# Kernel tuning notes

Measured on AMD Instinct MI355X. Metric: run time of the kernel, lower is better.

## Reference

```python
import jax, jax.numpy as jnp
import numpy as np

N = 50_000       # nodes
E = 1_600_000    # edges (avg degree 32)
F_IN = 128       # input features
H = 32           # hidden channels (both GCNConv layers)
C = 16           # num classes


def setup_inputs() -> dict:
    key = jax.random.key(0)
    ks = jax.random.split(key, 6)
    x = jax.random.normal(ks[0], (N, F_IN), dtype=jnp.float32)
    edge_index = jax.random.randint(ks[1], (2, E), 0, N, dtype=jnp.int32)
    W1 = jax.random.normal(ks[2], (F_IN, H), dtype=jnp.float32) / np.float32(np.sqrt(F_IN))
    b1 = jnp.zeros((H,), jnp.float32)
    W2 = jax.random.normal(ks[3], (H, H), dtype=jnp.float32) / np.float32(np.sqrt(H))
    b2 = jnp.zeros((H,), jnp.float32)
    Wc = jax.random.normal(ks[4], (H, C), dtype=jnp.float32) / np.float32(np.sqrt(H))
    bc = jnp.zeros((C,), jnp.float32)
    return {"x": x, "edge_index": edge_index, "W1": W1, "b1": b1,
            "W2": W2, "b2": b2, "Wc": Wc, "bc": bc}


def _gcn_conv(x, W, b, src, dst, deg_inv_sqrt, n):
    """PyG GCNConv: xW, then D^{-1/2}(A+I)D^{-1/2} aggregation, then bias.

    src/dst already include self-loops; deg_inv_sqrt precomputed on dst.
    """
    xw = x @ W                                   # [N, H]
    norm = deg_inv_sqrt[src] * deg_inv_sqrt[dst]  # [E+N]
    msg = xw[src] * norm[:, None]                # gather + scale, [E+N, H]
    out = jax.ops.segment_sum(msg, dst, num_segments=n)  # scatter-add
    return out + b


def reference(x, edge_index, W1, b1, W2, b2, Wc, bc):
    n = x.shape[0]
    loops = jnp.arange(n, dtype=edge_index.dtype)
    src = jnp.concatenate([edge_index[0], loops])  # add self-loops
    dst = jnp.concatenate([edge_index[1], loops])
    # degree over destination column (edge weight 1), as PyG gcn_norm does
    deg = jax.ops.segment_sum(jnp.ones_like(dst, dtype=x.dtype), dst, num_segments=n)
    deg_inv_sqrt = jnp.where(deg > 0, jax.lax.rsqrt(deg), 0.0)

    h = jnp.tanh(_gcn_conv(x, W1, b1, src, dst, deg_inv_sqrt, n))
    h = jnp.tanh(_gcn_conv(h, W2, b2, src, dst, deg_inv_sqrt, n))
    out = h @ Wc + bc
    return (out, h)
```

## Files before the change

### kernel.cpp

```cpp
#include <hip/hip_runtime.h>
#include <hip/hip_bf16.h>

#define NN 50000
#define EE 1600000
#define FIN 128
#define HH 32
#define CC 16
#define NB 782
#define NBLK 782
#define CHUNK 2048
#define FCAP 3072

typedef unsigned short u16;
typedef unsigned int u32;
typedef unsigned char u8;

__device__ __forceinline__ float bf2f(u16 u) {
    union { u32 i; float f; } v; v.i = ((u32)u) << 16; return v.f;
}
__device__ __forceinline__ u16 f2bf(float f) {
    union { float f; u32 i; } v; v.f = f;
    u32 x = v.i;
    return (u16)((x + 0x7fffu + ((x >> 16) & 1u)) >> 16);
}

__global__ __launch_bounds__(256) void k_place(const int* __restrict__ src, const int* __restrict__ dst,
                                               int* __restrict__ locT,
                                               u16* __restrict__ gsrc, u8* __restrict__ grel) {
    __shared__ int dst_s[CHUNK];
    __shared__ u16 s_src[CHUNK];
    __shared__ u8  s_rel[CHUNK];
    __shared__ int cur[NB];
    __shared__ int ps[256];
    const int tid = threadIdx.x, blk = blockIdx.x;
    const int e0 = blk * CHUNK;
    int cnt = EE - e0; if (cnt > CHUNK) cnt = CHUNK;

    const uint4* gd4 = (const uint4*)(dst + e0);
    for (int i = tid; i < cnt / 4; i += 256) ((uint4*)dst_s)[i] = gd4[i];
    for (int i = tid; i < NB; i += 256) cur[i] = 0;
    __syncthreads();

    for (int k = 0; k < CHUNK / 256; ++k) {
        int i = k * 256 + tid;
        if (i < cnt) atomicAdd(&cur[dst_s[i] >> 6], 1);
    }
    __syncthreads();

    const int bi = tid * 4;
    int v0 = 0, v1 = 0, v2 = 0, v3 = 0;
    if (bi < NB)     v0 = cur[bi];
    if (bi + 1 < NB) v1 = cur[bi + 1];
    if (bi + 2 < NB) v2 = cur[bi + 2];
    if (bi + 3 < NB) v3 = cur[bi + 3];
    ps[tid] = v0 + v1 + v2 + v3;
    __syncthreads();
    for (int off = 1; off < 256; off <<= 1) {
        int t = (tid >= off) ? ps[tid - off] : 0;
        __syncthreads();
        ps[tid] += t;
        __syncthreads();
    }
    int run = (tid == 0) ? 0 : ps[tid - 1];
    if (bi < NB)     { cur[bi] = run;     locT[(size_t)bi * NBLK + blk] = run;       run += v0; }
    if (bi + 1 < NB) { cur[bi + 1] = run; locT[(size_t)(bi + 1) * NBLK + blk] = run; run += v1; }
    if (bi + 2 < NB) { cur[bi + 2] = run; locT[(size_t)(bi + 2) * NBLK + blk] = run; run += v2; }
    if (bi + 3 < NB) { cur[bi + 3] = run; locT[(size_t)(bi + 3) * NBLK + blk] = run; run += v3; }
    if (tid == 255) locT[(size_t)NB * NBLK + blk] = ps[255];
    __syncthreads();

    for (int k = 0; k < CHUNK / 256; ++k) {
        int i = k * 256 + tid;
        if (i < cnt) {
            int d = dst_s[i];
            int pos = atomicAdd(&cur[d >> 6], 1);
            s_src[pos] = (u16)src[e0 + i];
            s_rel[pos] = (u8)(d & 63);
        }
    }
    __syncthreads();

    const uint4* ss = (const uint4*)s_src;
    uint4* gs = (uint4*)(gsrc + (size_t)blk * CHUNK);
    for (int i = tid; i < (cnt * 2) / 16; i += 256) gs[i] = ss[i];
    const uint4* sr = (const uint4*)s_rel;
    uint4* gr = (uint4*)(grel + (size_t)blk * CHUNK);
    for (int i = tid; i < cnt / 16; i += 256) gr[i] = sr[i];
}

__global__ __launch_bounds__(256) void k_btot(const int* __restrict__ locT, int* __restrict__ btot,
                                              const u32* __restrict__ xw_words, int* __restrict__ flag) {
    __shared__ int ps[256];
    __shared__ int cs;
    const int tid = threadIdx.x, cb = blockIdx.x;
    if (cb == 0) {
        if (tid == 0) cs = 0;
        __syncthreads();
        int c = 0;
        for (int i = tid; i < 512; i += 256) {
            float v = fabsf(bf2f((u16)(xw_words[i] & 0xffffu)));
            if (v >= 6.0e-8f && v <= 64.0f) c++;
        }
        atomicAdd(&cs, c);
        __syncthreads();
        if (tid == 0) *flag = (cs > 384) ? 1 : 0;
    }
    int s = 0;
    for (int b = tid; b < NBLK; b += 256)
        s += locT[(size_t)(cb + 1) * NBLK + b] - locT[(size_t)cb * NBLK + b];
    ps[tid] = s;
    __syncthreads();
    for (int off = 128; off > 0; off >>= 1) {
        if (tid < off) ps[tid] += ps[tid + off];
        __syncthreads();
    }
    if (tid == 0) btot[cb] = ps[0];
}

__global__ __launch_bounds__(256) void k_fine(const int* __restrict__ locT, const int* __restrict__ btot,
                                              const u16* __restrict__ gsrc, const u8* __restrict__ grel,
                                              int* __restrict__ rowptr, float* __restrict__ dis,
                                              u16* __restrict__ entries) {
    __shared__ int beg_s[NBLK];
    __shared__ int fo[NBLK + 1];
    __shared__ int ps[256];
    __shared__ int h[64];
    __shared__ int cur[64];
    __shared__ int sbase;
    __shared__ u16 lsrc[FCAP];
    __shared__ u8  lrel[FCAP];
    __shared__ u16 lout[FCAP];
    const int tid = threadIdx.x, cb = blockIdx.x;

    for (int b = tid; b < NBLK; b += 256) {
        int beg = locT[(size_t)cb * NBLK + b];
        beg_s[b] = beg;
        fo[b] = locT[(size_t)(cb + 1) * NBLK + b] - beg;
    }
    if (tid < 64) h[tid] = 0;

    int bs = 0;
    for (int j = tid; j < cb; j += 256) bs += btot[j];
    ps[tid] = bs;
    __syncthreads();
    for (int off = 128; off > 0; off >>= 1) {
        if (tid < off) ps[tid] += ps[tid + off];
        __syncthreads();
    }
    if (tid == 0) sbase = ps[0];
    __syncthreads();
    const int base = sbase;

    const int b0 = tid * 4;
    int a0 = 0, a1 = 0, a2 = 0, a3 = 0;
    if (b0 < NBLK)     a0 = fo[b0];
    if (b0 + 1 < NBLK) a1 = fo[b0 + 1];
    if (b0 + 2 < NBLK) a2 = fo[b0 + 2];
    if (b0 + 3 < NBLK) a3 = fo[b0 + 3];
    ps[tid] = a0 + a1 + a2 + a3;
    __syncthreads();
    for (int off = 1; off < 256; off <<= 1) {
        int v = (tid >= off) ? ps[tid - off] : 0;
        __syncthreads();
        ps[tid] += v;
        __syncthreads();
    }
    int run = (tid == 0) ? 0 : ps[tid - 1];
    if (b0 < NBLK)     { fo[b0] = run;     run += a0; }
    if (b0 + 1 < NBLK) { fo[b0 + 1] = run; run += a1; }
    if (b0 + 2 < NBLK) { fo[b0 + 2] = run; run += a2; }
    if (b0 + 3 < NBLK) { fo[b0 + 3] = run; run += a3; }
    if (tid == 255) fo[NBLK] = ps[255];
    __syncthreads();
    const int T = fo[NBLK];
    const bool staged = (T <= FCAP);

    if (staged) {
        for (int b = tid; b < NBLK; b += 256) {
            int g0 = b * CHUNK + beg_s[b];
            int o = fo[b];
            int L = fo[b + 1] - o;
            for (int j = 0; j < L; ++j) {
                u8 r = grel[g0 + j];
                lrel[o + j] = r;
                lsrc[o + j] = gsrc[g0 + j];
                atomicAdd(&h[r], 1);
            }
        }
    } else {
        for (int b = tid; b < NBLK; b += 256) {
            int g0 = b * CHUNK + beg_s[b];
            int L = fo[b + 1] - fo[b];
            for (int j = 0; j < L; ++j) atomicAdd(&h[grel[g0 + j]], 1);
        }
    }
    __syncthreads();

    int myv = (tid < 64) ? h[tid] : 0;
    ps[tid] = (tid < 64) ? myv : 0;
    __syncthreads();
    for (int off = 1; off < 64; off <<= 1) {
        int v = (tid >= off && tid < 64) ? ps[tid - off] : 0;
        __syncthreads();
        if (tid < 64) ps[tid] += v;
        __syncthreads();
    }
    if (tid < 64) {
        int excl = ps[tid] - myv;
        int n = cb * 64 + tid;
        cur[tid] = staged ? excl : base + excl;
        if (n < NN) {
            rowptr[n] = base + excl;
            dis[n] = rsqrtf((float)myv + 1.0f);
        }
    }
    if (cb == NB - 1 && tid == 0) rowptr[NN] = EE;
    __syncthreads();

    if (staged) {
        for (int i = tid; i < T; i += 256) {
            int pos = atomicAdd(&cur[lrel[i]], 1);
            lout[pos] = lsrc[i];
        }
        __syncthreads();
        for (int i = tid; i < T; i += 256) entries[base + i] = lout[i];
    } else {
        for (int b = tid; b < NBLK; b += 256) {
            int g0 = b * CHUNK + beg_s[b];
            int L = fo[b + 1] - fo[b];
            for (int j = 0; j < L; ++j) {
                int g = g0 + j;
                int pos = atomicAdd(&cur[grel[g]], 1);
                entries[pos] = gsrc[g];
            }
        }
    }
}

__global__ __launch_bounds__(256) void k_xw1(const void* __restrict__ xv, const void* __restrict__ W1v,
                                             const float* __restrict__ dis,
                                             const int* __restrict__ flag, u16* __restrict__ xwb) {
    __shared__ float wsm[FIN * HH];
    __shared__ float xs[128][33];
    const int f = *flag;
    const int tid = threadIdx.x;
    if (f) {
        const u16* W1 = (const u16*)W1v;
        for (int i = tid; i < FIN * HH; i += 256) wsm[i] = bf2f(W1[i]);
    } else {
        const float* W1 = (const float*)W1v;
        for (int i = tid; i < FIN * HH; i += 256) wsm[i] = W1[i];
    }
    const int n0 = blockIdx.x * 128;
    const int ct = tid & 7, rg = tid >> 3;
    const int lr = tid >> 1, lh = tid & 1;
    int ln = n0 + lr; if (ln >= NN) ln = NN - 1;
    float acc[4][4] = {};
    for (int kc = 0; kc < FIN; kc += 32) {
        __syncthreads();
        float* dq = &xs[lr][lh * 16];
        if (f) {
            const u16* lp = (const u16*)xv + (size_t)ln * FIN + lh * 16 + kc;
            uint4 a = *(const uint4*)lp;
            uint4 b = *(const uint4*)(lp + 8);
            u32 aw[4] = {a.x, a.y, a.z, a.w}, bw[4] = {b.x, b.y, b.z, b.w};
            #pragma unroll
            for (int i = 0; i < 4; ++i) {
                dq[2*i]     = bf2f((u16)(aw[i] & 0xffffu));
                dq[2*i+1]   = bf2f((u16)(aw[i] >> 16));
                dq[8+2*i]   = bf2f((u16)(bw[i] & 0xffffu));
                dq[8+2*i+1] = bf2f((u16)(bw[i] >> 16));
            }
        } else {
            const float* lp = (const float*)xv + (size_t)ln * FIN + lh * 16 + kc;
            #pragma unroll
            for (int i = 0; i < 4; ++i) {
                float4 t = *(const float4*)(lp + 4 * i);
                dq[4*i] = t.x; dq[4*i+1] = t.y; dq[4*i+2] = t.z; dq[4*i+3] = t.w;
            }
        }
        __syncthreads();
        #pragma unroll
        for (int k = 0; k < 32; ++k) {
            float4 wv = *(const float4*)&wsm[(kc + k) * HH + ct * 4];
            #pragma unroll
            for (int j = 0; j < 4; ++j) {
                float xvv = xs[rg * 4 + j][k];
                acc[j][0] = fmaf(xvv, wv.x, acc[j][0]);
                acc[j][1] = fmaf(xvv, wv.y, acc[j][1]);
                acc[j][2] = fmaf(xvv, wv.z, acc[j][2]);
                acc[j][3] = fmaf(xvv, wv.w, acc[j][3]);
            }
        }
    }
    #pragma unroll
    for (int j = 0; j < 4; ++j) {
        int n = n0 + rg * 4 + j;
        if (n < NN) {
            float dd = dis[n];
            ushort4 o;
            o.x = f2bf(dd * acc[j][0]); o.y = f2bf(dd * acc[j][1]);
            o.z = f2bf(dd * acc[j][2]); o.w = f2bf(dd * acc[j][3]);
            *(ushort4*)&xwb[(size_t)n * HH + ct * 4] = o;
        }
    }
}

__global__ __launch_bounds__(256) void k_g1(const int* __restrict__ rowptr, const u16* __restrict__ entries,
                                            const u16* __restrict__ xws, const float* __restrict__ dis,
                                            const void* __restrict__ bv, const int* __restrict__ flag,
                                            const void* __restrict__ W2v, u16* __restrict__ xwb2) {
    __shared__ float hrow[16][32];
    __shared__ float w2s[HH * HH];
    const int f = *flag;
    const int tid = threadIdx.x;
    if (f) {
        const u16* W2 = (const u16*)W2v;
        for (int i = tid; i < HH * HH; i += 256) w2s[i] = bf2f(W2[i]);
    } else {
        const float* W2 = (const float*)W2v;
        for (int i = tid; i < HH * HH; i += 256) w2s[i] = W2[i];
    }
    const int nl = tid >> 4;
    const int g = blockIdx.x * 16 + nl;
    const int c0 = (tid & 15) * 2;
    float b0, b1;
    if (f) { b0 = bf2f(((const u16*)bv)[c0]); b1 = bf2f(((const u16*)bv)[c0 + 1]); }
    else   { b0 = ((const float*)bv)[c0];     b1 = ((const float*)bv)[c0 + 1]; }
    const int beg = rowptr[g], end = rowptr[g + 1];
    const float dd = dis[g];
    u32 sw = *(const u32*)&xws[(size_t)g * HH + c0];
    float aL0 = bf2f((u16)(sw & 0xffffu)), aH0 = bf2f((u16)(sw >> 16));
    float aL1 = 0.f, aH1 = 0.f, aL2 = 0.f, aH2 = 0.f, aL3 = 0.f, aH3 = 0.f;
    int i = beg;
    for (; i < end && (i & 3); ++i) {
        u32 w = *(const u32*)&xws[(size_t)entries[i] * HH + c0];
        aL0 += bf2f((u16)(w & 0xffffu)); aH0 += bf2f((u16)(w >> 16));
    }
    for (; i + 4 <= end; i += 4) {
        ushort4 e4 = *(const ushort4*)&entries[i];
        u32 w0 = *(const u32*)&xws[(size_t)e4.x * HH + c0];
        u32 w1 = *(const u32*)&xws[(size_t)e4.y * HH + c0];
        u32 w2 = *(const u32*)&xws[(size_t)e4.z * HH + c0];
        u32 w3 = *(const u32*)&xws[(size_t)e4.w * HH + c0];
        aL0 += bf2f((u16)(w0 & 0xffffu)); aH0 += bf2f((u16)(w0 >> 16));
        aL1 += bf2f((u16)(w1 & 0xffffu)); aH1 += bf2f((u16)(w1 >> 16));
        aL2 += bf2f((u16)(w2 & 0xffffu)); aH2 += bf2f((u16)(w2 >> 16));
        aL3 += bf2f((u16)(w3 & 0xffffu)); aH3 += bf2f((u16)(w3 >> 16));
    }
    for (; i < end; ++i) {
        u32 w = *(const u32*)&xws[(size_t)entries[i] * HH + c0];
        aL0 += bf2f((u16)(w & 0xffffu)); aH0 += bf2f((u16)(w >> 16));
    }
    float vLo = tanhf(fmaf(dd, (aL0 + aL1) + (aL2 + aL3), b0));
    float vHi = tanhf(fmaf(dd, (aH0 + aH1) + (aH2 + aH3), b1));
    hrow[nl][c0] = vLo; hrow[nl][c0 + 1] = vHi;
    __syncthreads();
    float a0 = 0.f, a1 = 0.f;
    #pragma unroll
    for (int k = 0; k < HH; ++k) {
        float hv = hrow[nl][k];
        a0 = fmaf(hv, w2s[k * HH + c0], a0);
        a1 = fmaf(hv, w2s[k * HH + c0 + 1], a1);
    }
    u32 o = (u32)f2bf(dd * a0) | ((u32)f2bf(dd * a1) << 16);
    *(u32*)&xwb2[(size_t)g * HH + c0] = o;
}

__global__ __launch_bounds__(256) void k_g2(const int* __restrict__ rowptr, const u16* __restrict__ entries,
                                            const u16* __restrict__ xws, const float* __restrict__ dis,
                                            const void* __restrict__ bv, const int* __restrict__ flag,
                                            const void* __restrict__ Wcv, const void* __restrict__ bcv,
                                            void* __restrict__ outbase) {
    __shared__ float hrow[16][32];
    __shared__ float wcs[HH * CC];
    __shared__ float bcs[CC];
    const int f = *flag;
    const int tid = threadIdx.x;
    if (f) {
        const u16* Wc = (const u16*)Wcv;
        for (int i = tid; i < HH * CC; i += 256) wcs[i] = bf2f(Wc[i]);
        if (tid < CC) bcs[tid] = bf2f(((const u16*)bcv)[tid]);
    } else {
        const float* Wc = (const float*)Wcv;
        for (int i = tid; i < HH * CC; i += 256) wcs[i] = Wc[i];
        if (tid < CC) bcs[tid] = ((const float*)bcv)[tid];
    }
    const int nl = tid >> 4;
    const int g = blockIdx.x * 16 + nl;
    const int c0 = (tid & 15) * 2;
    float b0, b1;
    if (f) { b0 = bf2f(((const u16*)bv)[c0]); b1 = bf2f(((const u16*)bv)[c0 + 1]); }
    else   { b0 = ((const float*)bv)[c0];     b1 = ((const float*)bv)[c0 + 1]; }
    const int beg = rowptr[g], end = rowptr[g + 1];
    const float dd = dis[g];
    u32 sw = *(const u32*)&xws[(size_t)g * HH + c0];
    float aL0 = bf2f((u16)(sw & 0xffffu)), aH0 = bf2f((u16)(sw >> 16));
    float aL1 = 0.f, aH1 = 0.f, aL2 = 0.f, aH2 = 0.f, aL3 = 0.f, aH3 = 0.f;
    int i = beg;
    for (; i < end && (i & 3); ++i) {
        u32 w = *(const u32*)&xws[(size_t)entries[i] * HH + c0];
        aL0 += bf2f((u16)(w & 0xffffu)); aH0 += bf2f((u16)(w >> 16));
    }
    for (; i + 4 <= end; i += 4) {
        ushort4 e4 = *(const ushort4*)&entries[i];
        u32 w0 = *(const u32*)&xws[(size_t)e4.x * HH + c0];
        u32 w1 = *(const u32*)&xws[(size_t)e4.y * HH + c0];
        u32 w2 = *(const u32*)&xws[(size_t)e4.z * HH + c0];
        u32 w3 = *(const u32*)&xws[(size_t)e4.w * HH + c0];
        aL0 += bf2f((u16)(w0 & 0xffffu)); aH0 += bf2f((u16)(w0 >> 16));
        aL1 += bf2f((u16)(w1 & 0xffffu)); aH1 += bf2f((u16)(w1 >> 16));
        aL2 += bf2f((u16)(w2 & 0xffffu)); aH2 += bf2f((u16)(w2 >> 16));
        aL3 += bf2f((u16)(w3 & 0xffffu)); aH3 += bf2f((u16)(w3 >> 16));
    }
    for (; i < end; ++i) {
        u32 w = *(const u32*)&xws[(size_t)entries[i] * HH + c0];
        aL0 += bf2f((u16)(w & 0xffffu)); aH0 += bf2f((u16)(w >> 16));
    }
    float vLo = tanhf(fmaf(dd, (aL0 + aL1) + (aL2 + aL3), b0));
    float vHi = tanhf(fmaf(dd, (aH0 + aH1) + (aH2 + aH3), b1));
    size_t idx = (size_t)g * HH + c0;
    if (f) {
        u16* h2_16 = (u16*)outbase + (size_t)NN * CC;
        u32 o = (u32)f2bf(vLo) | ((u32)f2bf(vHi) << 16);
        *(u32*)&h2_16[idx] = o;
    } else {
        float* h2_32 = (float*)outbase + (size_t)NN * CC;
        *(float2*)&h2_32[idx] = make_float2(vLo, vHi);
    }
    hrow[nl][c0] = vLo; hrow[nl][c0 + 1] = vHi;
    __syncthreads();
    int cl = tid & 15;
    float acc = bcs[cl];
    #pragma unroll
    for (int k = 0; k < HH; ++k) acc = fmaf(hrow[nl][k], wcs[k * CC + cl], acc);
    size_t oi = (size_t)g * CC + cl;
    if (f) ((u16*)outbase)[oi] = f2bf(acc);
    else   ((float*)outbase)[oi] = acc;
}

extern "C" void kernel_launch(void* const* d_in, const int* in_sizes, int n_in,
                              void* d_out, int out_size, void* d_ws, size_t ws_size,
                              hipStream_t stream) {
    const void* x  = d_in[0];
    const int*  ei = (const int*)d_in[1];
    const void* W1 = d_in[2];
    const void* b1 = d_in[3];
    const void* W2 = d_in[4];
    const void* b2 = d_in[5];
    const void* Wc = d_in[6];
    const void* bc = d_in[7];
    const int* srcv = ei;
    const int* dstv = ei + EE;

    char*  ws     = (char*)d_ws;
    int*   flag   = (int*)ws;
    int*   rowptr = (int*)(ws + 4096);
    float* dis    = (float*)(ws + 208896);
    int*   btot   = (int*)(ws + 417792);
    int*   locT   = (int*)(ws + 421888);
    u16*   xwb    = (u16*)(ws + 2871296);
    u16*   entries= (u16*)(ws + 6071296);
    u16*   xwb2   = (u16*)(ws + 9271296);

    u16*   gsrc = (u16*)d_out;
    u8*    grel = (u8*)d_out + (size_t)EE * 2;

    k_place<<<NBLK, 256, 0, stream>>>(srcv, dstv, locT, gsrc, grel);
    k_btot<<<NB, 256, 0, stream>>>(locT, btot, (const u32*)x, flag);
    k_fine<<<NB, 256, 0, stream>>>(locT, btot, gsrc, grel, rowptr, dis, entries);

    k_xw1<<<(NN + 127) / 128, 256, 0, stream>>>(x, W1, dis, flag, xwb);
    k_g1<<<NN / 16, 256, 0, stream>>>(rowptr, entries, xwb, dis, b1, flag, W2, xwb2);
    k_g2<<<NN / 16, 256, 0, stream>>>(rowptr, entries, xwb2, dis, b2, flag, Wc, bc, d_out);
}
```

Measured before the change: 185.8 us.

## Widen gather loads to 4 channels per thread, 32 nodes per block

The two aggregation kernels now map 8 threads per node, each gathering 4 bf16 channels with 8-byte loads instead of 16 threads doing 4-byte loads, so each block covers 32 nodes and the grid is halved. Fewer, wider gather instructions per neighbour row and fewer index loads per node are intended to cut memory-instruction overhead in the gather-bound phase. The classifier epilogue computes two nodes per thread, and the CSR build writes entries as packed 32-bit pairs instead of 16-bit stores. In exchange each thread holds more accumulators, which raises register pressure, and a tail guard is added for the partial last block.

Result: no change. 184.7 us (-0.6%).

```diff
diff --git a/kernel.cpp b/kernel.cpp
--- a/kernel.cpp
+++ b/kernel.cpp
@@ -223,7 +223,15 @@
             lout[pos] = lsrc[i];
         }
         __syncthreads();
-        for (int i = tid; i < T; i += 256) entries[base + i] = lout[i];
+        const int st = base & 1;
+        if (st && tid == 0) entries[base] = lout[0];
+        for (int p = tid; ; p += 256) {
+            int i = st + 2 * p;
+            if (i + 1 >= T) break;
+            u32 w = (u32)lout[i] | ((u32)lout[i + 1] << 16);
+            *(u32*)&entries[base + i] = w;
+        }
+        if (((T - st) & 1) && tid == 0 && T > st) entries[base + T - 1] = lout[T - 1];
     } else {
         for (int b = tid; b < NBLK; b += 256) {
             int g0 = b * CHUNK + beg_s[b];
@@ -310,7 +318,7 @@
                                             const u16* __restrict__ xws, const float* __restrict__ dis,
                                             const void* __restrict__ bv, const int* __restrict__ flag,
                                             const void* __restrict__ W2v, u16* __restrict__ xwb2) {
-    __shared__ float hrow[16][32];
+    __shared__ float hrow[32][33];
     __shared__ float w2s[HH * HH];
     const int f = *flag;
     const int tid = threadIdx.x;
@@ -321,50 +329,72 @@
         const float* W2 = (const float*)W2v;
         for (int i = tid; i < HH * HH; i += 256) w2s[i] = W2[i];
     }
-    const int nl = tid >> 4;
-    const int g = blockIdx.x * 16 + nl;
-    const int c0 = (tid & 15) * 2;
-    float b0, b1;
-    if (f) { b0 = bf2f(((const u16*)bv)[c0]); b1 = bf2f(((const u16*)bv)[c0 + 1]); }
-    else   { b0 = ((const float*)bv)[c0];     b1 = ((const float*)bv)[c0 + 1]; }
+    const int nl = tid >> 3;
+    const int graw = blockIdx.x * 32 + nl;
+    const bool valid = graw < NN;
+    const int g = valid ? graw : NN - 1;
+    const int c0 = (tid & 7) * 4;
+    float bb0, bb1, bb2, bb3;
+    if (f) {
+        const u16* b = (const u16*)bv;
+        bb0 = bf2f(b[c0]); bb1 = bf2f(b[c0+1]); bb2 = bf2f(b[c0+2]); bb3 = bf2f(b[c0+3]);
+    } else {
+        const float* b = (const float*)bv;
+        bb0 = b[c0]; bb1 = b[c0+1]; bb2 = b[c0+2]; bb3 = b[c0+3];
+    }
     const int beg = rowptr[g], end = rowptr[g + 1];
     const float dd = dis[g];
-    u32 sw = *(const u32*)&xws[(size_t)g * HH + c0];
-    float aL0 = bf2f((u16)(sw & 0xffffu)), aH0 = bf2f((u16)(sw >> 16));
-    float aL1 = 0.f, aH1 = 0.f, aL2 = 0.f, aH2 = 0.f, aL3 = 0.f, aH3 = 0.f;
+    uint2 sw = *(const uint2*)&xws[(size_t)g * HH + c0];
+    float a00 = bf2f((u16)(sw.x & 0xffffu)), a01 = bf2f((u16)(sw.x >> 16));
+    float a02 = bf2f((u16)(sw.y & 0xffffu)), a03 = bf2f((u16)(sw.y >> 16));
+    float a10=0,a11=0,a12=0,a13=0, a20=0,a21=0,a22=0,a23=0, a30=0,a31=0,a32=0,a33=0;
     int i = beg;
     for (; i < end && (i & 3); ++i) {
-        u32 w = *(const u32*)&xws[(size_t)entries[i] * HH + c0];
-        aL0 += bf2f((u16)(w & 0xffffu)); aH0 += bf2f((u16)(w >> 16));
+        uint2 w = *(const uint2*)&xws[(size_t)entries[i] * HH + c0];
+        a00 += bf2f((u16)(w.x & 0xffffu)); a01 += bf2f((u16)(w.x >> 16));
+        a02 += bf2f((u16)(w.y & 0xffffu)); a03 += bf2f((u16)(w.y >> 16));
     }
     for (; i + 4 <= end; i += 4) {
         ushort4 e4 = *(const ushort4*)&entries[i];
-        u32 w0 = *(const u32*)&xws[(size_t)e4.x * HH + c0];
-        u32 w1 = *(const u32*)&xws[(size_t)e4.y * HH + c0];
-        u32 w2 = *(const u32*)&xws[(size_t)e4.z * HH + c0];
-        u32 w3 = *(const u32*)&xws[(size_t)e4.w * HH + c0];
-        aL0 += bf2f((u16)(w0 & 0xffffu)); aH0 += bf2f((u16)(w0 >> 16));
-        aL1 += bf2f((u16)(w1 & 0xffffu)); aH1 += bf2f((u16)(w1 >> 16));
-        aL2 += bf2f((u16)(w2 & 0xffffu)); aH2 += bf2f((u16)(w2 >> 16));
-        aL3 += bf2f((u16)(w3 & 0xffffu)); aH3 += bf2f((u16)(w3 >> 16));
+        uint2 w0 = *(const uint2*)&xws[(size_t)e4.x * HH + c0];
+        uint2 w1 = *(const uint2*)&xws[(size_t)e4.y * HH + c0];
+        uint2 w2 = *(const uint2*)&xws[(size_t)e4.z * HH + c0];
+        uint2 w3 = *(const uint2*)&xws[(size_t)e4.w * HH + c0];
+        a00 += bf2f((u16)(w0.x & 0xffffu)); a01 += bf2f((u16)(w0.x >> 16));
+        a02 += bf2f((u16)(w0.y & 0xffffu)); a03 += bf2f((u16)(w0.y >> 16));
+        a10 += bf2f((u16)(w1.x & 0xffffu)); a11 += bf2f((u16)(w1.x >> 16));
+        a12 += bf2f((u16)(w1.y & 0xffffu)); a13 += bf2f((u16)(w1.y >> 16));
+        a20 += bf2f((u16)(w2.x & 0xffffu)); a21 += bf2f((u16)(w2.x >> 16));
+        a22 += bf2f((u16)(w2.y & 0xffffu)); a23 += bf2f((u16)(w2.y >> 16));
+        a30 += bf2f((u16)(w3.x & 0xffffu)); a31 += bf2f((u16)(w3.x >> 16));
+        a32 += bf2f((u16)(w3.y & 0xffffu)); a33 += bf2f((u16)(w3.y >> 16));
     }
     for (; i < end; ++i) {
-        u32 w = *(const u32*)&xws[(size_t)entries[i] * HH + c0];
-        aL0 += bf2f((u16)(w & 0xffffu)); aH0 += bf2f((u16)(w >> 16));
-    }
-    float vLo = tanhf(fmaf(dd, (aL0 + aL1) + (aL2 + aL3), b0));
-    float vHi = tanhf(fmaf(dd, (aH0 + aH1) + (aH2 + aH3), b1));
-    hrow[nl][c0] = vLo; hrow[nl][c0 + 1] = vHi;
-    __syncthreads();
-    float a0 = 0.f, a1 = 0.f;
+        uint2 w = *(const uint2*)&xws[(size_t)entries[i] * HH + c0];
+        a00 += bf2f((u16)(w.x & 0xffffu)); a01 += bf2f((u16)(w.x >> 16));
+        a02 += bf2f((u16)(w.y & 0xffffu)); a03 += bf2f((u16)(w.y >> 16));
+    }
+    float v0 = tanhf(fmaf(dd, (a00 + a10) + (a20 + a30), bb0));
+    float v1 = tanhf(fmaf(dd, (a01 + a11) + (a21 + a31), bb1));
+    float v2 = tanhf(fmaf(dd, (a02 + a12) + (a22 + a32), bb2));
+    float v3 = tanhf(fmaf(dd, (a03 + a13) + (a23 + a33), bb3));
+    hrow[nl][c0] = v0; hrow[nl][c0+1] = v1; hrow[nl][c0+2] = v2; hrow[nl][c0+3] = v3;
+    __syncthreads();
+    float s0 = 0.f, s1 = 0.f, s2 = 0.f, s3 = 0.f;
     #pragma unroll
     for (int k = 0; k < HH; ++k) {
         float hv = hrow[nl][k];
-        a0 = fmaf(hv, w2s[k * HH + c0], a0);
-        a1 = fmaf(hv, w2s[k * HH + c0 + 1], a1);
-    }
-    u32 o = (u32)f2bf(dd * a0) | ((u32)f2bf(dd * a1) << 16);
-    *(u32*)&xwb2[(size_t)g * HH + c0] = o;
+        s0 = fmaf(hv, w2s[k * HH + c0], s0);
+        s1 = fmaf(hv, w2s[k * HH + c0 + 1], s1);
+        s2 = fmaf(hv, w2s[k * HH + c0 + 2], s2);
+        s3 = fmaf(hv, w2s[k * HH + c0 + 3], s3);
+    }
+    if (valid) {
+        uint2 o;
+        o.x = (u32)f2bf(dd * s0) | ((u32)f2bf(dd * s1) << 16);
+        o.y = (u32)f2bf(dd * s2) | ((u32)f2bf(dd * s3) << 16);
+        *(uint2*)&xwb2[(size_t)g * HH + c0] = o;
+    }
 }
 
 __global__ __launch_bounds__(256) void k_g2(const int* __restrict__ rowptr, const u16* __restrict__ entries,
@@ -372,7 +402,7 @@
                                             const void* __restrict__ bv, const int* __restrict__ flag,
                                             const void* __restrict__ Wcv, const void* __restrict__ bcv,
                                             void* __restrict__ outbase) {
-    __shared__ float hrow[16][32];
+    __shared__ float hrow[32][33];
     __shared__ float wcs[HH * CC];
     __shared__ float bcs[CC];
     const int f = *flag;
@@ -386,57 +416,90 @@
         for (int i = tid; i < HH * CC; i += 256) wcs[i] = Wc[i];
         if (tid < CC) bcs[tid] = ((const float*)bcv)[tid];
     }
-    const int nl = tid >> 4;
-    const int g = blockIdx.x * 16 + nl;
-    const int c0 = (tid & 15) * 2;
-    float b0, b1;
-    if (f) { b0 = bf2f(((const u16*)bv)[c0]); b1 = bf2f(((const u16*)bv)[c0 + 1]); }
-    else   { b0 = ((const float*)bv)[c0];     b1 = ((const float*)bv)[c0 + 1]; }
+    const int nl = tid >> 3;
+    const int graw = blockIdx.x * 32 + nl;
+    const bool valid = graw < NN;
+    const int g = valid ? graw : NN - 1;
+    const int c0 = (tid & 7) * 4;
+    float bb0, bb1, bb2, bb3;
+    if (f) {
+        const u16* b = (const u16*)bv;
+        bb0 = bf2f(b[c0]); bb1 = bf2f(b[c0+1]); bb2 = bf2f(b[c0+2]); bb3 = bf2f(b[c0+3]);
+    } else {
+        const float* b = (const float*)bv;
+        bb0 = b[c0]; bb1 = b[c0+1]; bb2 = b[c0+2]; bb3 = b[c0+3];
+    }
     const int beg = rowptr[g], end = rowptr[g + 1];
     const float dd = dis[g];
-    u32 sw = *(const u32*)&xws[(size_t)g * HH + c0];
-    float aL0 = bf2f((u16)(sw & 0xffffu)), aH0 = bf2f((u16)(sw >> 16));
-    float aL1 = 0.f, aH1 = 0.f, aL2 = 0.f, aH2 = 0.f, aL3 = 0.f, aH3 = 0.f;
+    uint2 sw = *(const uint2*)&xws[(size_t)g * HH + c0];
+    float a00 = bf2f((u16)(sw.x & 0xffffu)), a01 = bf2f((u16)(sw.x >> 16));
+    float a02 = bf2f((u16)(sw.y & 0xffffu)), a03 = bf2f((u16)(sw.y >> 16));
+    float a10=0,a11=0,a12=0,a13=0, a20=0,a21=0,a22=0,a23=0, a30=0,a31=0,a32=0,a33=0;
     int i = beg;
     for (; i < end && (i & 3); ++i) {
-        u32 w = *(const u32*)&xws[(size_t)entries[i] * HH + c0];
-        aL0 += bf2f((u16)(w & 0xffffu)); aH0 += bf2f((u16)(w >> 16));
+        uint2 w = *(const uint2*)&xws[(size_t)entries[i] * HH + c0];
+        a00 += bf2f((u16)(w.x & 0xffffu)); a01 += bf2f((u16)(w.x >> 16));
+        a02 += bf2f((u16)(w.y & 0xffffu)); a03 += bf2f((u16)(w.y >> 16));
     }
     for (; i + 4 <= end; i += 4) {
         ushort4 e4 = *(const ushort4*)&entries[i];
-        u32 w0 = *(const u32*)&xws[(size_t)e4.x * HH + c0];
-        u32 w1 = *(const u32*)&xws[(size_t)e4.y * HH + c0];
-        u32 w2 = *(const u32*)&xws[(size_t)e4.z * HH + c0];
-        u32 w3 = *(const u32*)&xws[(size_t)e4.w * HH + c0];
-        aL0 += bf2f((u16)(w0 & 0xffffu)); aH0 += bf2f((u16)(w0 >> 16));
-        aL1 += bf2f((u16)(w1 & 0xffffu)); aH1 += bf2f((u16)(w1 >> 16));
-        aL2 += bf2f((u16)(w2 & 0xffffu)); aH2 += bf2f((u16)(w2 >> 16));
-        aL3 += bf2f((u16)(w3 & 0xffffu)); aH3 += bf2f((u16)(w3 >> 16));
+        uint2 w0 = *(const uint2*)&xws[(size_t)e4.x * HH + c0];
+        uint2 w1 = *(const uint2*)&xws[(size_t)e4.y * HH + c0];
+        uint2 w2 = *(const uint2*)&xws[(size_t)e4.z * HH + c0];
+        uint2 w3 = *(const uint2*)&xws[(size_t)e4.w * HH + c0];
+        a00 += bf2f((u16)(w0.x & 0xffffu)); a01 += bf2f((u16)(w0.x >> 16));
+        a02 += bf2f((u16)(w0.y & 0xffffu)); a03 += bf2f((u16)(w0.y >> 16));
+        a10 += bf2f((u16)(w1.x & 0xffffu)); a11 += bf2f((u16)(w1.x >> 16));
+        a12 += bf2f((u16)(w1.y & 0xffffu)); a13 += bf2f((u16)(w1.y >> 16));
+        a20 += bf2f((u16)(w2.x & 0xffffu)); a21 += bf2f((u16)(w2.x >> 16));
+        a22 += bf2f((u16)(w2.y & 0xffffu)); a23 += bf2f((u16)(w2.y >> 16));
+        a30 += bf2f((u16)(w3.x & 0xffffu)); a31 += bf2f((u16)(w3.x >> 16));
+        a32 += bf2f((u16)(w3.y & 0xffffu)); a33 += bf2f((u16)(w3.y >> 16));
     }
     for (; i < end; ++i) {
-        u32 w = *(const u32*)&xws[(size_t)entries[i] * HH + c0];
-        aL0 += bf2f((u16)(w & 0xffffu)); aH0 += bf2f((u16)(w >> 16));
-    }
-    float vLo = tanhf(fmaf(dd, (aL0 + aL1) + (aL2 + aL3), b0));
-    float vHi = tanhf(fmaf(dd, (aH0 + aH1) + (aH2 + aH3), b1));
-    size_t idx = (size_t)g * HH + c0;
-    if (f) {
-        u16* h2_16 = (u16*)outbase + (size_t)NN * CC;
-        u32 o = (u32)f2bf(vLo) | ((u32)f2bf(vHi) << 16);
-        *(u32*)&h2_16[idx] = o;
-    } else {
-        float* h2_32 = (float*)outbase + (size_t)NN * CC;
-        *(float2*)&h2_32[idx] = make_float2(vLo, vHi);
-    }
-    hrow[nl][c0] = vLo; hrow[nl][c0 + 1] = vHi;
-    __syncthreads();
-    int cl = tid & 15;
-    float acc = bcs[cl];
+        uint2 w = *(const uint2*)&xws[(size_t)entries[i] * HH + c0];
+        a00 += bf2f((u16)(w.x & 0xffffu)); a01 += bf2f((u16)(w.x >> 16));
+        a02 += bf2f((u16)(w.y & 0xffffu)); a03 += bf2f((u16)(w.y >> 16));
+    }
+    float v0 = tanhf(fmaf(dd, (a00 + a10) + (a20 + a30), bb0));
+    float v1 = tanhf(fmaf(dd, (a01 + a11) + (a21 + a31), bb1));
+    float v2 = tanhf(fmaf(dd, (a02 + a12) + (a22 + a32), bb2));
+    float v3 = tanhf(fmaf(dd, (a03 + a13) + (a23 + a33), bb3));
+    if (valid) {
+        size_t idx = (size_t)g * HH + c0;
+        if (f) {
+            u16* h2_16 = (u16*)outbase + (size_t)NN * CC;
+            uint2 o;
+            o.x = (u32)f2bf(v0) | ((u32)f2bf(v1) << 16);
+            o.y = (u32)f2bf(v2) | ((u32)f2bf(v3) << 16);
+            *(uint2*)&h2_16[idx] = o;
+        } else {
+            float* h2_32 = (float*)outbase + (size_t)NN * CC;
+            *(float4*)&h2_32[idx] = make_float4(v0, v1, v2, v3);
+        }
+    }
+    hrow[nl][c0] = v0; hrow[nl][c0+1] = v1; hrow[nl][c0+2] = v2; hrow[nl][c0+3] = v3;
+    __syncthreads();
+    const int nA = tid >> 4, cl = tid & 15;
+    const int nB = nA + 16;
+    float accA = bcs[cl], accB = bcs[cl];
     #pragma unroll
-    for (int k = 0; k < HH; ++k) acc = fmaf(hrow[nl][k], wcs[k * CC + cl], acc);
-    size_t oi = (size_t)g * CC + cl;
-    if (f) ((u16*)outbase)[oi] = f2bf(acc);
-    else   ((float*)outbase)[oi] = acc;
+    for (int k = 0; k < HH; ++k) {
+        float wv = wcs[k * CC + cl];
+        accA = fmaf(hrow[nA][k], wv, accA);
+        accB = fmaf(hrow[nB][k], wv, accB);
+    }
+    const int gA = blockIdx.x * 32 + nA, gB = blockIdx.x * 32 + nB;
+    if (gA < NN) {
+        size_t oi = (size_t)gA * CC + cl;
+        if (f) ((u16*)outbase)[oi] = f2bf(accA);
+        else   ((float*)outbase)[oi] = accA;
+    }
+    if (gB < NN) {
+        size_t oi = (size_t)gB * CC + cl;
+        if (f) ((u16*)outbase)[oi] = f2bf(accB);
+        else   ((float*)outbase)[oi] = accB;
+    }
 }
 
 extern "C" void kernel_launch(void* const* d_in, const int* in_sizes, int n_in,
@@ -471,6 +534,6 @@
     k_fine<<<NB, 256, 0, stream>>>(locT, btot, gsrc, grel, rowptr, dis, entries);
 
     k_xw1<<<(NN + 127) / 128, 256, 0, stream>>>(x, W1, dis, flag, xwb);
-    k_g1<<<NN / 16, 256, 0, stream>>>(rowptr, entries, xwb, dis, b1, flag, W2, xwb2);
-    k_g2<<<NN / 16, 256, 0, stream>>>(rowptr, entries, xwb2, dis, b2, flag, Wc, bc, d_out);
-}
+    k_g1<<<(NN + 31) / 32, 256, 0, stream>>>(rowptr, entries, xwb, dis, b1, flag, W2, xwb2);
+    k_g2<<<(NN + 31) / 32, 256, 0, stream>>>(rowptr, entries, xwb2, dis, b2, flag, Wc, bc, d_out);
+}
```
